# Kernel optimization log

Hardware: AMD Instinct MI355X
Metric: run time of the kernel (lower is better)

Reference implementation:

```python
import jax, jax.numpy as jnp
import numpy as np

N_P, N_A, D, E = 200000, 100000, 256, 1000000


def setup_inputs() -> dict:
    key = jax.random.key(0)
    ks = jax.random.split(key, 6)
    return {
        "x_paper": jax.random.normal(ks[0], (N_P, D), dtype=jnp.float32),
        "x_author": jax.random.normal(ks[1], (N_A, D), dtype=jnp.float32),
        # relation ('paper','to','author'): src in [0,N_P), dst in [0,N_A)
        "e_pa_src": jax.random.randint(ks[2], (E,), 0, N_P),
        "e_pa_dst": jax.random.randint(ks[3], (E,), 0, N_A),
        # relation ('author','to','paper'): src in [0,N_A), dst in [0,N_P)
        "e_ap_src": jax.random.randint(ks[4], (E,), 0, N_A),
        "e_ap_dst": jax.random.randint(ks[5], (E,), 0, N_P),
    }


def reference(x_paper, x_author, e_pa_src, e_pa_dst, e_ap_src, e_ap_dst):
    n_author = x_author.shape[0]  # x_dict['author'] supplies dst size for hop 1
    n_paper = x_paper.shape[0]
    # Hop 1: conv over ('paper','to','author'): gather x_paper at edge src,
    # scatter-sum to author dst, then per-dict relu (norm=False => plain x_j messages).
    x_a1 = jax.nn.relu(
        jax.ops.segment_sum(x_paper[e_pa_src], e_pa_dst, num_segments=n_author)
    )
    # Hop 2: conv over ('author','to','paper') reads the updated author features.
    x_p2 = jax.nn.relu(
        jax.ops.segment_sum(x_a1[e_ap_src], e_ap_dst, num_segments=n_paper)
    )
    # collect_mode=False -> return x_dict[metapath[0]] == updated paper features
    return x_p2
```

## Files before the change

### kernel.cpp

```cpp
#include <hip/hip_runtime.h>

#define DIM 256
#define RPB 32
#define LOG_RPB 5
#define NG 8
#define CAP 128
#define BCAP 512
#define PC_B 3072

typedef float f32x4 __attribute__((ext_vector_type(4)));
typedef unsigned int u32;
typedef unsigned short u16;

__device__ __forceinline__ u16 f32_to_bf16_rne(float f) {
    u32 u = __float_as_uint(f);
    return (u16)((u + 0x7FFFu + ((u >> 16) & 1u)) >> 16);
}


__global__ void place_conv(const int* __restrict__ sA, const int* __restrict__ dA,
                           const int* __restrict__ sB, const int* __restrict__ dB,
                           int* __restrict__ cnt, u32* __restrict__ binned,
                           int TBc, int NBA_, int E1, int Etot,
                           const float* __restrict__ xin, u16* __restrict__ xbf,
                           long long n4) {
    int grp = (int)blockIdx.x >> 3;
    int lane8 = (int)blockIdx.x & 7;
    if (grp % 3 == 0) {
        int sub = (grp / 3) * 8 + lane8;
        int nplace = ((int)gridDim.x / 24) * 8;
        int stride = nplace * (int)blockDim.x;
        for (int e = sub * (int)blockDim.x + (int)threadIdx.x; e < Etot; e += stride) {
            int g = (e >> 8) & (NG - 1);
            int s, d, b;
            if (e < E1) {
                s = __builtin_nontemporal_load(sA + e);
                d = __builtin_nontemporal_load(dA + e);
                b = d >> LOG_RPB;
            } else {
                int e2 = e - E1;
                s = __builtin_nontemporal_load(sB + e2);
                d = __builtin_nontemporal_load(dB + e2);
                b = NBA_ + (d >> LOG_RPB);
            }
            int cell = g * TBc + b;
            int old = atomicAdd(&cnt[cell], 1);
            if (old < CAP)
                binned[(long long)cell * CAP + old] = ((u32)s << LOG_RPB) | (u32)(d & (RPB - 1));
        }
    } else {
        int cg = grp - (grp / 3 + 1);
        int sub = cg * 8 + lane8;
        long long nconv = ((long long)gridDim.x / 24) * 16;
        long long stride = nconv * blockDim.x;
        for (long long i = (long long)sub * blockDim.x + threadIdx.x; i < n4; i += stride) {
            f32x4 v = __builtin_nontemporal_load((const f32x4*)xin + i);
            ushort4 o;
            o.x = f32_to_bf16_rne(v.x); o.y = f32_to_bf16_rne(v.y);
            o.z = f32_to_bf16_rne(v.z); o.w = f32_to_bf16_rne(v.w);
            *((ushort4*)xbf + i) = o;
        }
    }
}


template <int BATCH, bool DBF>
__global__ void __launch_bounds__(256)
gather_hop(const u32* __restrict__ binned, const int* __restrict__ cnt,
           const u16* __restrict__ xv, void* __restrict__ outv,
           int TBc, int bucket_base, int n) {
    __shared__ int sed[BCAP];
    __shared__ int rp[RPB + 1];
    __shared__ int c[RPB];
    __shared__ int cur[RPB];

    int tid = (int)threadIdx.x;
    int b = bucket_base + (int)blockIdx.x;

    if (tid < RPB) c[tid] = 0;
    __syncthreads();
#pragma unroll
    for (int g = 0; g < NG; ++g) {
        int cell = g * TBc + b;
        int m = cnt[cell]; m = (m < CAP) ? m : CAP;
        long long base = (long long)cell * CAP;
        for (int i = tid; i < m; i += 256)
            atomicAdd(&c[binned[base + i] & (RPB - 1)], 1);
    }
    __syncthreads();
    if (tid == 0) {
        int run = 0;
        for (int r = 0; r < RPB; ++r) { cur[r] = run; rp[r] = run; run += c[r]; }
        rp[RPB] = run;
    }
    __syncthreads();
#pragma unroll
    for (int g = 0; g < NG; ++g) {
        int cell = g * TBc + b;
        int m = cnt[cell]; m = (m < CAP) ? m : CAP;
        long long base = (long long)cell * CAP;
        for (int i = tid; i < m; i += 256) {
            u32 e = binned[base + i];
            int pos = atomicAdd(&cur[e & (RPB - 1)], 1);
            sed[pos] = (int)(e >> LOG_RPB);
        }
    }
    __syncthreads();

    int lane = tid & 63, w = tid >> 6;
    int row0 = (int)blockIdx.x * RPB;
    for (int rr = w; rr < RPB; rr += 4) {
        int row = row0 + rr;
        if (row >= n) break;
        int beg = rp[rr];
        int end = rp[rr + 1];
        float ax = 0.f, ay = 0.f, az = 0.f, aw = 0.f;
        for (int i = beg; i < end; i += BATCH) {
            int m = end - i;
            m = (m < BATCH) ? m : BATCH;
            uint2 vv[BATCH];
#pragma unroll
            for (int j = 0; j < BATCH; ++j) {
                int jj = (j < m) ? j : (m - 1);
                int s = sed[i + jj];
                vv[j] = *((const uint2*)(xv + (long long)s * DIM) + lane);
            }
#pragma unroll
            for (int j = 0; j < BATCH; ++j) {
                float mk = (j < m) ? 1.0f : 0.0f;
                ax = fmaf(mk, __uint_as_float(vv[j].x << 16), ax);
                ay = fmaf(mk, __uint_as_float(vv[j].x & 0xFFFF0000u), ay);
                az = fmaf(mk, __uint_as_float(vv[j].y << 16), az);
                aw = fmaf(mk, __uint_as_float(vv[j].y & 0xFFFF0000u), aw);
            }
        }
        ax = fmaxf(ax, 0.f); ay = fmaxf(ay, 0.f); az = fmaxf(az, 0.f); aw = fmaxf(aw, 0.f);
        if (DBF) {
            ushort4 o;
            o.x = f32_to_bf16_rne(ax); o.y = f32_to_bf16_rne(ay);
            o.z = f32_to_bf16_rne(az); o.w = f32_to_bf16_rne(aw);
            *((ushort4*)outv + (long long)row * (DIM / 4) + lane) = o;
        } else {
            f32x4 o = { ax, ay, az, aw };
            __builtin_nontemporal_store(o, (f32x4*)outv + (long long)row * (DIM / 4) + lane);
        }
    }
}


extern "C" void kernel_launch(void* const* d_in, const int* in_sizes, int n_in,
                              void* d_out, int out_size, void* d_ws, size_t ws_size,
                              hipStream_t stream) {
    const float* x_paper = (const float*)d_in[0];
    const int* e_pa_src = (const int*)d_in[2];
    const int* e_pa_dst = (const int*)d_in[3];
    const int* e_ap_src = (const int*)d_in[4];
    const int* e_ap_dst = (const int*)d_in[5];

    const int nA = in_sizes[1] / DIM;
    const int nB = in_sizes[0] / DIM;
    const int E1 = in_sizes[2];
    const int E2 = in_sizes[4];
    const int Etot = E1 + E2;

    const int NBA = (nA + RPB - 1) / RPB;
    const int NBB = (nB + RPB - 1) / RPB;
    const int TBc = NBA + NBB;

    size_t off = 0;
    auto alloc = [&](size_t bytes) { size_t o = off; off += (bytes + 255) & ~(size_t)255; return o; };
    size_t o_xpbf   = alloc((size_t)nB * DIM * sizeof(u16));
    size_t o_xa1    = alloc((size_t)nA * DIM * sizeof(u16));
    size_t o_cnt    = alloc((size_t)NG * TBc * sizeof(int));
    size_t o_binned = alloc((size_t)NG * TBc * CAP * sizeof(u32));
    (void)ws_size;

    char* ws = (char*)d_ws;
    u16* xpbf   = (u16*)(ws + o_xpbf);
    u16* x_a1   = (u16*)(ws + o_xa1);
    int* cnt    = (int*)(ws + o_cnt);
    u32* binned = (u32*)(ws + o_binned);
    float* x_p2 = (float*)d_out;

    hipMemsetAsync(cnt, 0, (size_t)NG * TBc * sizeof(int), stream);

    long long n4 = (long long)nB * DIM / 4;
    place_conv<<<PC_B, 256, 0, stream>>>(
        e_pa_src, e_pa_dst, e_ap_src, e_ap_dst, cnt, binned,
        TBc, NBA, E1, Etot, x_paper, xpbf, n4);

    gather_hop<16, true><<<NBA, 256, 0, stream>>>(binned, cnt, xpbf, x_a1, TBc, 0, nA);

    gather_hop<8, false><<<NBB, 256, 0, stream>>>(binned, cnt, x_a1, x_p2, TBc, NBA, nB);
}
```

Measured before the change: 297.7 us.

## Stage binned edges in shared memory once and rebalance place/convert block split

The gather kernel now reads each bucket's binned edges from global memory once into a shared staging buffer, computing per-group offsets first. Both the counting pass and the scatter pass then work from shared memory instead of reading global memory twice. The place_conv kernel also moves from a 1:2 to a 1:3 split between edge-placing and bf16-conversion blocks, giving conversion more blocks. The cost is an extra 2KB of shared memory and an extra barrier per block.

```diff
diff --git a/kernel.cpp b/kernel.cpp
--- a/kernel.cpp
+++ b/kernel.cpp
@@ -26,9 +26,9 @@
                            long long n4) {
     int grp = (int)blockIdx.x >> 3;
     int lane8 = (int)blockIdx.x & 7;
-    if (grp % 3 == 0) {
-        int sub = (grp / 3) * 8 + lane8;
-        int nplace = ((int)gridDim.x / 24) * 8;
+    if ((grp & 3) == 0) {
+        int sub = (grp >> 2) * 8 + lane8;
+        int nplace = ((int)gridDim.x >> 5) * 8;
         int stride = nplace * (int)blockDim.x;
         for (int e = sub * (int)blockDim.x + (int)threadIdx.x; e < Etot; e += stride) {
             int g = (e >> 8) & (NG - 1);
@@ -49,9 +49,9 @@
                 binned[(long long)cell * CAP + old] = ((u32)s << LOG_RPB) | (u32)(d & (RPB - 1));
         }
     } else {
-        int cg = grp - (grp / 3 + 1);
+        int cg = grp - ((grp >> 2) + 1);
         int sub = cg * 8 + lane8;
-        long long nconv = ((long long)gridDim.x / 24) * 16;
+        long long nconv = ((long long)gridDim.x >> 5) * 24;
         long long stride = nconv * blockDim.x;
         for (long long i = (long long)sub * blockDim.x + threadIdx.x; i < n4; i += stride) {
             f32x4 v = __builtin_nontemporal_load((const f32x4*)xin + i);
@@ -69,24 +69,39 @@
 gather_hop(const u32* __restrict__ binned, const int* __restrict__ cnt,
            const u16* __restrict__ xv, void* __restrict__ outv,
            int TBc, int bucket_base, int n) {
+    __shared__ int stage[BCAP];
     __shared__ int sed[BCAP];
     __shared__ int rp[RPB + 1];
     __shared__ int c[RPB];
     __shared__ int cur[RPB];
+    __shared__ int ofs[NG + 1];
 
     int tid = (int)threadIdx.x;
     int b = bucket_base + (int)blockIdx.x;
 
+    if (tid < NG) {
+        int m = cnt[tid * TBc + b];
+        ofs[tid + 1] = (m < CAP) ? m : CAP;
+    }
     if (tid < RPB) c[tid] = 0;
     __syncthreads();
+    if (tid == 0) {
+        ofs[0] = 0;
+#pragma unroll
+        for (int g = 0; g < NG; ++g) ofs[g + 1] += ofs[g];
+    }
+    __syncthreads();
 #pragma unroll
     for (int g = 0; g < NG; ++g) {
-        int cell = g * TBc + b;
-        int m = cnt[cell]; m = (m < CAP) ? m : CAP;
-        long long base = (long long)cell * CAP;
+        int o0 = ofs[g], m = ofs[g + 1] - o0;
+        long long base = (long long)(g * TBc + b) * CAP;
         for (int i = tid; i < m; i += 256)
-            atomicAdd(&c[binned[base + i] & (RPB - 1)], 1);
-    }
+            stage[o0 + i] = (int)binned[base + i];
+    }
+    __syncthreads();
+    int tot = ofs[NG];
+    for (int i = tid; i < tot; i += 256)
+        atomicAdd(&c[stage[i] & (RPB - 1)], 1);
     __syncthreads();
     if (tid == 0) {
         int run = 0;
@@ -94,16 +109,10 @@
         rp[RPB] = run;
     }
     __syncthreads();
-#pragma unroll
-    for (int g = 0; g < NG; ++g) {
-        int cell = g * TBc + b;
-        int m = cnt[cell]; m = (m < CAP) ? m : CAP;
-        long long base = (long long)cell * CAP;
-        for (int i = tid; i < m; i += 256) {
-            u32 e = binned[base + i];
-            int pos = atomicAdd(&cur[e & (RPB - 1)], 1);
-            sed[pos] = (int)(e >> LOG_RPB);
-        }
+    for (int i = tid; i < tot; i += 256) {
+        u32 e = (u32)stage[i];
+        int pos = atomicAdd(&cur[e & (RPB - 1)], 1);
+        sed[pos] = (int)(e >> LOG_RPB);
     }
     __syncthreads();
 
```

Measured after the change: 334.4 us. 12.3% more time.
